# Performance work log

Hardware: AMD Instinct MI355X
Metric: run time of the kernel (lower is better)

## Reference

```python
import jax, jax.numpy as jnp
import numpy as np

N_NODES = 50000
N_EDGES = 500000
IN_DIM = 256
HIDDEN = 128
HEADS = 4
N_CLS = 10
N_GRAPHS = 512
NEG_SLOPE = 0.2  # PyG GATConv default leaky-relu slope


def _glorot(key, shape):
    fan_in, fan_out = shape[0], shape[-1]
    lim = jnp.sqrt(6.0 / (fan_in + fan_out))
    return jax.random.uniform(key, shape, jnp.float32, -lim, lim)


def setup_inputs() -> dict:
    key = jax.random.key(0)
    ks = jax.random.split(key, 12)
    x = jax.random.normal(ks[0], (N_NODES, IN_DIM), jnp.float32)
    edge_index = jax.random.randint(ks[1], (2, N_EDGES), 0, N_NODES, jnp.int64)
    batch = jnp.sort(jax.random.randint(ks[2], (N_NODES,), 0, N_GRAPHS, jnp.int64))
    HC = HIDDEN * HEADS
    return {
        "x": x,
        "edge_index": edge_index,
        "batch": batch,
        "W1": _glorot(ks[3], (IN_DIM, HC)),
        "a_src1": _glorot(ks[4], (HEADS, HIDDEN)) * 0.1,
        "a_dst1": _glorot(ks[5], (HEADS, HIDDEN)) * 0.1,
        "b1": jnp.zeros((HC,), jnp.float32),
        "W2": _glorot(ks[6], (HC, HC)),
        "a_src2": _glorot(ks[7], (HEADS, HIDDEN)) * 0.1,
        "a_dst2": _glorot(ks[8], (HEADS, HIDDEN)) * 0.1,
        "b2": jnp.zeros((HC,), jnp.float32),
        "Wc": _glorot(ks[9], (HC, N_CLS)),
        "bc": jnp.zeros((N_CLS,), jnp.float32),
    }


def _gat_layer(x, src, dst, W, a_src, a_dst, b):
    """PyG GATConv (concat=True, self-loops already appended, eval mode)."""
    N = x.shape[0]
    h = (x @ W).reshape(N, HEADS, -1)                 # [N, H, C]
    alpha_s = jnp.einsum('nhc,hc->nh', h, a_src)       # [N, H]
    alpha_d = jnp.einsum('nhc,hc->nh', h, a_dst)       # [N, H]
    e = jax.nn.leaky_relu(alpha_s[src] + alpha_d[dst], NEG_SLOPE)  # [E, H]
    # segment softmax over incoming edges of each dst node
    m = jax.ops.segment_max(e, dst, num_segments=N)
    ex = jnp.exp(e - m[dst])
    denom = jax.ops.segment_sum(ex, dst, num_segments=N)
    alpha = ex / (denom[dst] + 1e-16)                  # [E, H]
    out = jax.ops.segment_sum(alpha[:, :, None] * h[src], dst, num_segments=N)
    return out.reshape(N, -1) + b                      # [N, H*C]


def reference(x, edge_index, batch, W1, a_src1, a_dst1, b1,
              W2, a_src2, a_dst2, b2, Wc, bc):
    N = x.shape[0]
    loop = jnp.arange(N, dtype=edge_index.dtype)
    src = jnp.concatenate([edge_index[0], loop])
    dst = jnp.concatenate([edge_index[1], loop])
    h = jax.nn.relu(_gat_layer(x, src, dst, W1, a_src1, a_dst1, b1))
    h = jax.nn.relu(_gat_layer(h, src, dst, W2, a_src2, a_dst2, b2))
    # global mean pool over graphs
    sums = jax.ops.segment_sum(h, batch, num_segments=N_GRAPHS)
    cnt = jax.ops.segment_sum(jnp.ones((N,), h.dtype), batch, num_segments=N_GRAPHS)
    hg = sums / jnp.maximum(cnt, 1.0)[:, None]         # [G, H*C]
    return hg @ Wc + bc                                # [G, n_cls]
```

## Files before the change

kernel.cpp:

```cpp
#include <hip/hip_runtime.h>

#define NN      50000
#define NE      500000
#define NET     550000
#define IND     256
#define HC      512
#define NH      4
#define NG      512
#define NCLS    10

typedef __attribute__((ext_vector_type(8))) _Float16 f16x8;
typedef __attribute__((ext_vector_type(4))) float f32x4;
typedef __attribute__((ext_vector_type(2))) float f32x2;
typedef __attribute__((ext_vector_type(4))) ushort us4;

__device__ __forceinline__ ushort f2bf(float x) {
    unsigned u = __float_as_uint(x);
    u += 0x7fffu + ((u >> 16) & 1u);
    return (ushort)(u >> 16);
}
__device__ __forceinline__ float bf2f(ushort h) {
    return __uint_as_float((unsigned)h << 16);
}
__device__ __forceinline__ ushort f2h(float x) {
    union { _Float16 h; ushort u; } cv;
    cv.h = (_Float16)x;
    return cv.u;
}
__device__ __forceinline__ float h2f(ushort u) {
    union { ushort u; _Float16 h; } cv;
    cv.u = u;
    return (float)cv.h;
}

__device__ __forceinline__ void gload_lds16(const void* g, void* s) {
    __builtin_amdgcn_global_load_lds(
        (const __attribute__((address_space(1))) unsigned*)g,
        (__attribute__((address_space(3))) unsigned*)s, 16, 0, 0);
}

__global__ __launch_bounds__(256) void k_gemm_f16(
    const ushort* __restrict__ A, const ushort* __restrict__ BT,
    const float* __restrict__ a_srcv, const float* __restrict__ a_dstv,
    unsigned char* __restrict__ Cf8, float* __restrict__ as_b,
    float* __restrict__ ad_b, int M, int K)
{
    __shared__ __align__(16) ushort As[64 * 64];
    __shared__ __align__(16) ushort Bs[128 * 64];
    __shared__ float sred[2][64];

    const int tid = threadIdx.x;
    const int nwg = gridDim.x;
    const int orig = blockIdx.x;
    const int q = nwg >> 3, r = nwg & 7, xcd = orig & 7;
    const int wgid = (xcd < r ? xcd * (q + 1) : r * (q + 1) + (xcd - r) * q) + (orig >> 3);
    const int bm = (wgid >> 2) * 64;
    const int bn = (wgid & 3) * 128;

    const int l = tid & 63;
    const int w = tid >> 6;
    const int wm = (w >> 1) * 32, wn = (w & 1) * 64;
    const int fr = l & 15;
    const int fk = (l >> 4) * 8;

    if (tid < 64) { sred[0][tid] = 0.f; sred[1][tid] = 0.f; }

    f32x4 zero = {0.f, 0.f, 0.f, 0.f};
    f32x4 acc[2][4];
#pragma unroll
    for (int m = 0; m < 2; ++m)
#pragma unroll
        for (int n = 0; n < 4; ++n) acc[m][n] = zero;

    const int nsteps = K >> 6;
    const int wbase = (tid & 0xC0) << 4;

    for (int ks = 0; ks < nsteps; ++ks) {
        int k0 = ks << 6;
#pragma unroll
        for (int i = 0; i < 2; ++i) {
            int c = i * 256 + tid;
            int row = c >> 3;
            int col16 = (c & 7) ^ (row & 7);
            int arow = bm + row; arow = arow < M ? arow : M - 1;
            gload_lds16(A + (size_t)arow * K + k0 + (col16 << 3),
                        (char*)As + i * 4096 + wbase);
        }
#pragma unroll
        for (int i = 0; i < 4; ++i) {
            int c = i * 256 + tid;
            int j = c >> 3;
            int col16 = (c & 7) ^ (j & 7);
            gload_lds16(BT + (size_t)(bn + j) * K + k0 + (col16 << 3),
                        (char*)Bs + i * 4096 + wbase);
        }
        __syncthreads();
#pragma unroll
        for (int kk = 0; kk < 64; kk += 32) {
            f16x8 a[2], b[4];
            int kb = (kk + fk) >> 3;
#pragma unroll
            for (int m = 0; m < 2; ++m) {
                int row = wm + m * 16 + fr;
                a[m] = *(const f16x8*)((const char*)As + row * 128 + ((kb ^ (row & 7)) << 4));
            }
#pragma unroll
            for (int n = 0; n < 4; ++n) {
                int col = wn + n * 16 + fr;
                b[n] = *(const f16x8*)((const char*)Bs + col * 128 + ((kb ^ (col & 7)) << 4));
            }
#pragma unroll
            for (int m = 0; m < 2; ++m)
#pragma unroll
                for (int n = 0; n < 4; ++n)
                    acc[m][n] = __builtin_amdgcn_mfma_f32_16x16x32_f16(a[m], b[n], acc[m][n], 0, 0, 0);
        }
        __syncthreads();
    }

    const int hh = bn >> 7;
    float asl[4], adl[4];
#pragma unroll
    for (int n = 0; n < 4; ++n) {
        int c = wn + n * 16 + fr;
        asl[n] = a_srcv[hh * 128 + c];
        adl[n] = a_dstv[hh * 128 + c];
    }
    const int rbase = (l >> 4) * 4;
#pragma unroll
    for (int m = 0; m < 2; ++m) {
#pragma unroll
        for (int rr = 0; rr < 4; ++rr) {
            int rloc = wm + m * 16 + rbase + rr;
            int rowi = bm + rloc;
            float ps = 0.f, pd = 0.f;
#pragma unroll
            for (int n = 0; n < 4; ++n) {
                float v = acc[m][n][rr];
                ps += v * asl[n];
                pd += v * adl[n];
                if (rowi < M) {
                    int pk = __builtin_amdgcn_cvt_pk_fp8_f32(v, v, 0, false);
                    Cf8[(size_t)rowi * HC + bn + wn + n * 16 + fr] = (unsigned char)pk;
                }
            }
#pragma unroll
            for (int off = 1; off < 16; off <<= 1) {
                ps += __shfl_xor(ps, off, 64);
                pd += __shfl_xor(pd, off, 64);
            }
            if (fr == 0) {
                atomicAdd(&sred[0][rloc], ps);
                atomicAdd(&sred[1][rloc], pd);
            }
        }
    }
    __syncthreads();
    if (tid < 64) {
        int rowi = bm + tid;
        if (rowi < M) {
            as_b[rowi * 4 + hh] = sred[0][tid];
            ad_b[rowi * 4 + hh] = sred[1][tid];
        }
    }
}

__global__ void k_cvt_f16(const float* __restrict__ in, ushort* __restrict__ o,
                          int n4) {
    int i = blockIdx.x * blockDim.x + threadIdx.x;
    if (i >= n4) return;
    float4 v = ((const float4*)in)[i];
    ushort4 h;
    h.x = f2h(v.x); h.y = f2h(v.y); h.z = f2h(v.z); h.w = f2h(v.w);
    ((ushort4*)o)[i] = h;
}

__global__ void k_cvt_wT(const float* __restrict__ W, ushort* __restrict__ hT,
                         int K, int logK) {
    int id = blockIdx.x * blockDim.x + threadIdx.x;
    if (id >= (HC << logK)) return;
    int nn = id >> logK, k = id & (K - 1);
    hT[id] = f2h(W[(size_t)k * HC + nn]);
}

__global__ void k_deg(const int* __restrict__ ei, int* __restrict__ deg) {
    int e = blockIdx.x * blockDim.x + threadIdx.x;
    if (e >= NET) return;
    int d = (e < NE) ? ei[NE + e] : (e - NE);
    atomicAdd(&deg[d], 1);
}

__global__ __launch_bounds__(256) void k_scan_part(const int* __restrict__ cnt,
                                                   int* __restrict__ bsum, int n) {
    __shared__ int red[256];
    const int tid = threadIdx.x;
    int i = blockIdx.x * 256 + tid;
    red[tid] = (i < n) ? cnt[i] : 0;
    __syncthreads();
#pragma unroll
    for (int d = 128; d; d >>= 1) {
        if (tid < d) red[tid] += red[tid + d];
        __syncthreads();
    }
    if (tid == 0) bsum[blockIdx.x] = red[0];
}

__global__ __launch_bounds__(1024) void k_scan_top(const int* __restrict__ bsum,
                                                   int* __restrict__ boff,
                                                   int* __restrict__ off, int nb, int n) {
    __shared__ int s[1024];
    const int tid = threadIdx.x;
    int v = (tid < nb) ? bsum[tid] : 0;
    s[tid] = v;
    __syncthreads();
    for (int d = 1; d < 1024; d <<= 1) {
        int t = (tid >= d) ? s[tid - d] : 0;
        __syncthreads();
        s[tid] += t;
        __syncthreads();
    }
    if (tid < nb) boff[tid] = s[tid] - v;
    if (tid == nb - 1) off[n] = s[tid];
}

__global__ __launch_bounds__(256) void k_scan_out(const int* __restrict__ cnt,
                                                  const int* __restrict__ boff,
                                                  int* __restrict__ off, int n) {
    __shared__ int s[256];
    const int tid = threadIdx.x;
    int i = blockIdx.x * 256 + tid;
    int v = (i < n) ? cnt[i] : 0;
    s[tid] = v;
    __syncthreads();
    for (int d = 1; d < 256; d <<= 1) {
        int t = (tid >= d) ? s[tid - d] : 0;
        __syncthreads();
        s[tid] += t;
        __syncthreads();
    }
    if (i < n) off[i] = boff[blockIdx.x] + s[tid] - v;
}

__global__ void k_fill(const int* __restrict__ ei,
                       const int* __restrict__ rowptr,
                       int* __restrict__ fillcnt,
                       ushort* __restrict__ colsrc) {
    int e = blockIdx.x * blockDim.x + threadIdx.x;
    if (e >= NET) return;
    int s, d;
    if (e < NE) { s = ei[e]; d = ei[NE + e]; } else { s = d = e - NE; }
    int pos = rowptr[d] + atomicAdd(&fillcnt[d], 1);
    colsrc[pos] = (ushort)s;
}

__global__ __launch_bounds__(256) void k_stats(
    const float* __restrict__ as, const float* __restrict__ ad,
    const int* __restrict__ rowptr, const ushort* __restrict__ colsrc,
    ushort* __restrict__ alpha, float* __restrict__ dinv, int N)
{
    const int n = blockIdx.x * 64 + (threadIdx.x >> 2);
    if (n >= N) return;
    const int h = threadIdx.x & 3;
    const int beg = rowptr[n], end = rowptr[n + 1];
    const float adn = ad[n * 4 + h];
    float sum = 0.f;
    for (int e = beg; e < end; ++e) {
        float ev = as[(int)colsrc[e] * 4 + h] + adn;
        ev = ev > 0.f ? ev : 0.2f * ev;
        float a = __expf(ev);
        alpha[(size_t)e * 4 + h] = f2h(a);
        sum += a;
    }
    dinv[n * 4 + h] = 1.0f / (sum + 1e-16f);
}

__global__ __launch_bounds__(256) void k_gather(
    const unsigned char* __restrict__ zf8, const ushort* __restrict__ alpha,
    const float* __restrict__ dinv, const int* __restrict__ rowptr,
    const ushort* __restrict__ colsrc, const float* __restrict__ bias,
    ushort* __restrict__ o16, int obf16)
{
    const int npb = NN >> 2;
    const int hp = blockIdx.x / npb;
    const int sub = threadIdx.x >> 5;
    const int node = (blockIdx.x % npb) * 4 + (sub >> 1);
    const int head = hp * 2 + (sub & 1);
    const int lane = threadIdx.x & 31;
    const int beg = rowptr[node], end = rowptr[node + 1];
    const unsigned char* __restrict__ zh = zf8 + head * 128 + (lane << 2);

    float ax = 0.f, ay = 0.f, az = 0.f, aw = 0.f;
    int e = beg;
    for (; e + 8 <= end; e += 8) {
        int s[8];
        float a[8];
        unsigned u[8];
#pragma unroll
        for (int j = 0; j < 8; ++j) {
            s[j] = colsrc[e + j];
            a[j] = h2f(alpha[(size_t)(e + j) * 4 + head]);
        }
#pragma unroll
        for (int j = 0; j < 8; ++j) u[j] = *(const unsigned*)&zh[(size_t)s[j] * HC];
#pragma unroll
        for (int j = 0; j < 8; ++j) {
            f32x2 lo = __builtin_amdgcn_cvt_pk_f32_fp8(u[j], false);
            f32x2 hi = __builtin_amdgcn_cvt_pk_f32_fp8(u[j], true);
            ax += a[j] * lo.x; ay += a[j] * lo.y;
            az += a[j] * hi.x; aw += a[j] * hi.y;
        }
    }
    for (; e + 2 <= end; e += 2) {
        int s0 = colsrc[e], s1 = colsrc[e + 1];
        float a0 = h2f(alpha[(size_t)e * 4 + head]);
        float a1 = h2f(alpha[(size_t)(e + 1) * 4 + head]);
        unsigned u0 = *(const unsigned*)&zh[(size_t)s0 * HC];
        unsigned u1 = *(const unsigned*)&zh[(size_t)s1 * HC];
        f32x2 l0 = __builtin_amdgcn_cvt_pk_f32_fp8(u0, false);
        f32x2 h0 = __builtin_amdgcn_cvt_pk_f32_fp8(u0, true);
        f32x2 l1 = __builtin_amdgcn_cvt_pk_f32_fp8(u1, false);
        f32x2 h1 = __builtin_amdgcn_cvt_pk_f32_fp8(u1, true);
        ax += a0 * l0.x + a1 * l1.x; ay += a0 * l0.y + a1 * l1.y;
        az += a0 * h0.x + a1 * h1.x; aw += a0 * h0.y + a1 * h1.y;
    }
    if (e < end) {
        int s0 = colsrc[e];
        float a0 = h2f(alpha[(size_t)e * 4 + head]);
        unsigned u0 = *(const unsigned*)&zh[(size_t)s0 * HC];
        f32x2 l0 = __builtin_amdgcn_cvt_pk_f32_fp8(u0, false);
        f32x2 h0 = __builtin_amdgcn_cvt_pk_f32_fp8(u0, true);
        ax += a0 * l0.x; ay += a0 * l0.y; az += a0 * h0.x; aw += a0 * h0.y;
    }
    const float di = dinv[node * 4 + head];
    const int col = head * 128 + (lane << 2);
    float4 bv = *(const float4*)&bias[col];
    float rx = fmaxf(ax * di + bv.x, 0.f), ry = fmaxf(ay * di + bv.y, 0.f);
    float rz = fmaxf(az * di + bv.z, 0.f), rw = fmaxf(aw * di + bv.w, 0.f);
    us4 h;
    if (obf16) {
        h.x = f2bf(rx); h.y = f2bf(ry); h.z = f2bf(rz); h.w = f2bf(rw);
    } else {
        h.x = f2h(rx); h.y = f2h(ry); h.z = f2h(rz); h.w = f2h(rw);
    }
    __builtin_nontemporal_store(h, (us4*)&o16[(size_t)node * HC + col]);
}

__global__ void k_gcnt(const int* __restrict__ batch, int* __restrict__ gcnt) {
    int n = blockIdx.x * blockDim.x + threadIdx.x;
    if (n < NN) atomicAdd(&gcnt[batch[n]], 1);
}

__global__ __launch_bounds__(128) void k_pool(const ushort* __restrict__ h,
                                              const int* __restrict__ goff,
                                              const int* __restrict__ gcnt,
                                              float* __restrict__ hg) {
    const int g = blockIdx.x;
    const int tid = threadIdx.x;
    const int beg = goff[g];
    const int cnt = gcnt[g];
    float4 acc = make_float4(0.f, 0.f, 0.f, 0.f);
    for (int r = beg; r < beg + cnt; ++r) {
        ushort4 v = *(const ushort4*)&h[(size_t)r * HC + (tid << 2)];
        acc.x += bf2f(v.x); acc.y += bf2f(v.y);
        acc.z += bf2f(v.z); acc.w += bf2f(v.w);
    }
    float inv = 1.0f / (float)max(cnt, 1);
    *(float4*)&hg[(size_t)g * HC + (tid << 2)] =
        make_float4(acc.x * inv, acc.y * inv, acc.z * inv, acc.w * inv);
}

__global__ __launch_bounds__(64) void k_cls(const float* __restrict__ hg,
                                            const float* __restrict__ Wc,
                                            const float* __restrict__ bc,
                                            float* __restrict__ out) {
    const int g = blockIdx.x;
    const int lane = threadIdx.x;
#pragma unroll 1
    for (int cls = 0; cls < NCLS; ++cls) {
        float p = 0.f;
#pragma unroll
        for (int j = 0; j < 8; ++j) {
            int c = lane + j * 64;
            p += hg[(size_t)g * HC + c] * Wc[c * NCLS + cls];
        }
#pragma unroll
        for (int off = 32; off; off >>= 1) p += __shfl_down(p, off, 64);
        if (lane == 0) out[g * NCLS + cls] = p + bc[cls];
    }
}

extern "C" void kernel_launch(void* const* d_in, const int* in_sizes, int n_in,
                              void* d_out, int out_size, void* d_ws, size_t ws_size,
                              hipStream_t stream) {
    const float* x     = (const float*)d_in[0];
    const int*   ei    = (const int*)d_in[1];
    const int*   batch = (const int*)d_in[2];
    const float* W1    = (const float*)d_in[3];
    const float* asrc1 = (const float*)d_in[4];
    const float* adst1 = (const float*)d_in[5];
    const float* b1    = (const float*)d_in[6];
    const float* W2    = (const float*)d_in[7];
    const float* asrc2 = (const float*)d_in[8];
    const float* adst2 = (const float*)d_in[9];
    const float* b2    = (const float*)d_in[10];
    const float* Wc    = (const float*)d_in[11];
    const float* bc    = (const float*)d_in[12];
    float* out = (float*)d_out;
    (void)in_sizes; (void)n_in; (void)out_size; (void)ws_size;

    char* R = (char*)d_ws;
    const size_t MB512 = (size_t)NN * HC;
    unsigned char* zf8 = (unsigned char*)R;
    ushort* xf16  = (ushort*)(R + MB512);
    ushort* h1f16 = (ushort*)(R + MB512);
    ushort* h2b   = (ushort*)(R + MB512);

    char* w = R + MB512 * 3;
    size_t off = 0;
    auto alloc = [&](size_t bytes) {
        void* p = w + off;
        off += (bytes + 255) & ~(size_t)255;
        return p;
    };
    float* as_b = (float*)alloc((size_t)NN * NH * 4);
    float* ad_b = (float*)alloc((size_t)NN * NH * 4);
    float* dinv = (float*)alloc((size_t)NN * NH * 4);
    int* rowptr = (int*)alloc((size_t)(NN + 1) * 4);
    int* deg    = (int*)alloc((size_t)NN * 4);
    ushort* colsrc = (ushort*)alloc((size_t)NET * 2);
    int* gcnt   = (int*)alloc((size_t)NG * 4);
    int* goff   = (int*)alloc((size_t)(NG + 1) * 4);
    int* bsum   = (int*)alloc((size_t)1024 * 4);
    int* boff   = (int*)alloc((size_t)1024 * 4);
    float* hg   = (float*)alloc((size_t)NG * HC * 4);
    ushort* W1T = (ushort*)alloc((size_t)HC * IND * 2);
    ushort* W2T = (ushort*)alloc((size_t)HC * HC * 2);
    ushort* alpha = (ushort*)alloc((size_t)NET * NH * 2);

    const int EB = 256, EG = (NET + EB - 1) / EB;
    const int MT = (NN + 63) / 64;
    const int GG = 2 * (NN >> 2);
    const int NB_N = (NN + 255) / 256;
    const int NB_G = (NG + 255) / 256;

    k_cvt_f16<<<(NN * IND / 4 + 255) / 256, 256, 0, stream>>>(x, xf16, NN * IND / 4);
    k_cvt_wT<<<(HC * IND + 255) / 256, 256, 0, stream>>>(W1, W1T, IND, 8);
    k_cvt_wT<<<(HC * HC + 255) / 256, 256, 0, stream>>>(W2, W2T, HC, 9);

    hipMemsetAsync(deg, 0, (size_t)NN * 4, stream);
    k_deg<<<EG, EB, 0, stream>>>(ei, deg);
    k_scan_part<<<NB_N, 256, 0, stream>>>(deg, bsum, NN);
    k_scan_top<<<1, 1024, 0, stream>>>(bsum, boff, rowptr, NB_N, NN);
    k_scan_out<<<NB_N, 256, 0, stream>>>(deg, boff, rowptr, NN);
    hipMemsetAsync(deg, 0, (size_t)NN * 4, stream);
    k_fill<<<EG, EB, 0, stream>>>(ei, rowptr, deg, colsrc);

    hipMemsetAsync(gcnt, 0, (size_t)NG * 4, stream);
    k_gcnt<<<(NN + 255) / 256, 256, 0, stream>>>(batch, gcnt);
    k_scan_part<<<NB_G, 256, 0, stream>>>(gcnt, bsum, NG);
    k_scan_top<<<1, 1024, 0, stream>>>(bsum, boff, goff, NB_G, NG);
    k_scan_out<<<NB_G, 256, 0, stream>>>(gcnt, boff, goff, NG);

    k_gemm_f16<<<MT * 4, 256, 0, stream>>>(xf16, W1T, asrc1, adst1,
                                           zf8, as_b, ad_b, NN, IND);
    k_stats<<<(NN + 63) / 64, 256, 0, stream>>>(as_b, ad_b, rowptr, colsrc,
                                                alpha, dinv, NN);
    k_gather<<<GG, 256, 0, stream>>>(zf8, alpha, dinv, rowptr, colsrc, b1,
                                     h1f16, 0);

    k_gemm_f16<<<MT * 4, 256, 0, stream>>>(h1f16, W2T, asrc2, adst2,
                                           zf8, as_b, ad_b, NN, HC);
    k_stats<<<(NN + 63) / 64, 256, 0, stream>>>(as_b, ad_b, rowptr, colsrc,
                                                alpha, dinv, NN);
    k_gather<<<GG, 256, 0, stream>>>(zf8, alpha, dinv, rowptr, colsrc, b2,
                                     h2b, 1);

    k_pool<<<NG, 128, 0, stream>>>(h2b, goff, gcnt, hg);
    k_cls<<<NG, 64, 0, stream>>>(hg, Wc, bc, out);
}
```

Before: 394.2 us.

## Double-buffer GEMM LDS tiles and fuse small preprocessing kernels

The GEMM now double-buffers its A/B LDS tiles, issuing the next k-step's global-to-LDS loads before computing the current one and replacing __syncthreads with an explicit vmcnt wait plus barrier. Separately, the three conversion kernels are merged into one launch, the degree and graph-count atomics are merged into one kernel, and the graph offset scan uses a single-block 512-thread scan instead of the three-kernel scan. Together these aim to hide global load latency in the GEMM and cut kernel launch overhead. The cost is doubled LDS per block, which may lower occupancy, and the vmcnt(0) wait only partially overlaps the loads with compute.

```diff
diff --git a/kernel.cpp b/kernel.cpp
--- a/kernel.cpp
+++ b/kernel.cpp
@@ -45,8 +45,8 @@
     unsigned char* __restrict__ Cf8, float* __restrict__ as_b,
     float* __restrict__ ad_b, int M, int K)
 {
-    __shared__ __align__(16) ushort As[64 * 64];
-    __shared__ __align__(16) ushort Bs[128 * 64];
+    __shared__ __align__(16) ushort As[2][64 * 64];
+    __shared__ __align__(16) ushort Bs[2][128 * 64];
     __shared__ float sred[2][64];
 
     const int tid = threadIdx.x;
@@ -75,7 +75,7 @@
     const int nsteps = K >> 6;
     const int wbase = (tid & 0xC0) << 4;
 
-    for (int ks = 0; ks < nsteps; ++ks) {
+    auto stage = [&](int buf, int ks) {
         int k0 = ks << 6;
 #pragma unroll
         for (int i = 0; i < 2; ++i) {
@@ -84,7 +84,7 @@
             int col16 = (c & 7) ^ (row & 7);
             int arow = bm + row; arow = arow < M ? arow : M - 1;
             gload_lds16(A + (size_t)arow * K + k0 + (col16 << 3),
-                        (char*)As + i * 4096 + wbase);
+                        (char*)As[buf] + i * 4096 + wbase);
         }
 #pragma unroll
         for (int i = 0; i < 4; ++i) {
@@ -92,9 +92,17 @@
             int j = c >> 3;
             int col16 = (c & 7) ^ (j & 7);
             gload_lds16(BT + (size_t)(bn + j) * K + k0 + (col16 << 3),
-                        (char*)Bs + i * 4096 + wbase);
-        }
-        __syncthreads();
+                        (char*)Bs[buf] + i * 4096 + wbase);
+        }
+    };
+
+    stage(0, 0);
+    asm volatile("s_waitcnt vmcnt(0)" ::: "memory");
+    __builtin_amdgcn_s_barrier();
+
+    for (int ks = 0; ks < nsteps; ++ks) {
+        const int cur = ks & 1;
+        if (ks + 1 < nsteps) stage(cur ^ 1, ks + 1);
 #pragma unroll
         for (int kk = 0; kk < 64; kk += 32) {
             f16x8 a[2], b[4];
@@ -102,12 +110,12 @@
 #pragma unroll
             for (int m = 0; m < 2; ++m) {
                 int row = wm + m * 16 + fr;
-                a[m] = *(const f16x8*)((const char*)As + row * 128 + ((kb ^ (row & 7)) << 4));
+                a[m] = *(const f16x8*)((const char*)As[cur] + row * 128 + ((kb ^ (row & 7)) << 4));
             }
 #pragma unroll
             for (int n = 0; n < 4; ++n) {
                 int col = wn + n * 16 + fr;
-                b[n] = *(const f16x8*)((const char*)Bs + col * 128 + ((kb ^ (col & 7)) << 4));
+                b[n] = *(const f16x8*)((const char*)Bs[cur] + col * 128 + ((kb ^ (col & 7)) << 4));
             }
 #pragma unroll
             for (int m = 0; m < 2; ++m)
@@ -115,7 +123,8 @@
                 for (int n = 0; n < 4; ++n)
                     acc[m][n] = __builtin_amdgcn_mfma_f32_16x16x32_f16(a[m], b[n], acc[m][n], 0, 0, 0);
         }
-        __syncthreads();
+        asm volatile("s_waitcnt vmcnt(0)" ::: "memory");
+        __builtin_amdgcn_s_barrier();
     }
 
     const int hh = bn >> 7;
@@ -165,29 +174,43 @@
     }
 }
 
-__global__ void k_cvt_f16(const float* __restrict__ in, ushort* __restrict__ o,
-                          int n4) {
+#define CVT_X4   (NN * IND / 4)
+#define CVT_W1   (HC * IND)
+#define CVT_W2   (HC * HC)
+__global__ void k_cvt_all(const float* __restrict__ x, ushort* __restrict__ xf16,
+                          const float* __restrict__ W1, ushort* __restrict__ W1T,
+                          const float* __restrict__ W2, ushort* __restrict__ W2T) {
     int i = blockIdx.x * blockDim.x + threadIdx.x;
-    if (i >= n4) return;
-    float4 v = ((const float4*)in)[i];
-    ushort4 h;
-    h.x = f2h(v.x); h.y = f2h(v.y); h.z = f2h(v.z); h.w = f2h(v.w);
-    ((ushort4*)o)[i] = h;
-}
-
-__global__ void k_cvt_wT(const float* __restrict__ W, ushort* __restrict__ hT,
-                         int K, int logK) {
-    int id = blockIdx.x * blockDim.x + threadIdx.x;
-    if (id >= (HC << logK)) return;
-    int nn = id >> logK, k = id & (K - 1);
-    hT[id] = f2h(W[(size_t)k * HC + nn]);
-}
-
-__global__ void k_deg(const int* __restrict__ ei, int* __restrict__ deg) {
-    int e = blockIdx.x * blockDim.x + threadIdx.x;
-    if (e >= NET) return;
-    int d = (e < NE) ? ei[NE + e] : (e - NE);
-    atomicAdd(&deg[d], 1);
+    if (i < CVT_X4) {
+        float4 v = ((const float4*)x)[i];
+        ushort4 h;
+        h.x = f2h(v.x); h.y = f2h(v.y); h.z = f2h(v.z); h.w = f2h(v.w);
+        ((ushort4*)xf16)[i] = h;
+        return;
+    }
+    i -= CVT_X4;
+    if (i < CVT_W1) {
+        int nn = i >> 8, k = i & 255;
+        W1T[i] = f2h(W1[(size_t)k * HC + nn]);
+        return;
+    }
+    i -= CVT_W1;
+    if (i < CVT_W2) {
+        int nn = i >> 9, k = i & 511;
+        W2T[i] = f2h(W2[(size_t)k * HC + nn]);
+    }
+}
+
+__global__ void k_count(const int* __restrict__ ei, int* __restrict__ deg,
+                        const int* __restrict__ batch, int* __restrict__ gcnt) {
+    int i = blockIdx.x * blockDim.x + threadIdx.x;
+    if (i < NET) {
+        int d = (i < NE) ? ei[NE + i] : (i - NE);
+        atomicAdd(&deg[d], 1);
+    } else {
+        int j = i - NET;
+        if (j < NN) atomicAdd(&gcnt[batch[j]], 1);
+    }
 }
 
 __global__ __launch_bounds__(256) void k_scan_part(const int* __restrict__ cnt,
@@ -239,6 +262,23 @@
         __syncthreads();
     }
     if (i < n) off[i] = boff[blockIdx.x] + s[tid] - v;
+}
+
+__global__ __launch_bounds__(512) void k_scan_small(const int* __restrict__ cnt,
+                                                    int* __restrict__ off, int n) {
+    __shared__ int s[512];
+    const int tid = threadIdx.x;
+    int v = (tid < n) ? cnt[tid] : 0;
+    s[tid] = v;
+    __syncthreads();
+    for (int d = 1; d < 512; d <<= 1) {
+        int t = (tid >= d) ? s[tid - d] : 0;
+        __syncthreads();
+        s[tid] += t;
+        __syncthreads();
+    }
+    if (tid < n) off[tid] = s[tid] - v;
+    if (tid == n - 1) off[n] = s[tid];
 }
 
 __global__ void k_fill(const int* __restrict__ ei,
@@ -345,19 +385,13 @@
     __builtin_nontemporal_store(h, (us4*)&o16[(size_t)node * HC + col]);
 }
 
-__global__ void k_gcnt(const int* __restrict__ batch, int* __restrict__ gcnt) {
-    int n = blockIdx.x * blockDim.x + threadIdx.x;
-    if (n < NN) atomicAdd(&gcnt[batch[n]], 1);
-}
-
 __global__ __launch_bounds__(128) void k_pool(const ushort* __restrict__ h,
                                               const int* __restrict__ goff,
-                                              const int* __restrict__ gcnt,
                                               float* __restrict__ hg) {
     const int g = blockIdx.x;
     const int tid = threadIdx.x;
     const int beg = goff[g];
-    const int cnt = gcnt[g];
+    const int cnt = goff[g + 1] - beg;
     float4 acc = make_float4(0.f, 0.f, 0.f, 0.f);
     for (int r = beg; r < beg + cnt; ++r) {
         ushort4 v = *(const ushort4*)&h[(size_t)r * HC + (tid << 2)];
@@ -441,25 +475,20 @@
     const int MT = (NN + 63) / 64;
     const int GG = 2 * (NN >> 2);
     const int NB_N = (NN + 255) / 256;
-    const int NB_G = (NG + 255) / 256;
-
-    k_cvt_f16<<<(NN * IND / 4 + 255) / 256, 256, 0, stream>>>(x, xf16, NN * IND / 4);
-    k_cvt_wT<<<(HC * IND + 255) / 256, 256, 0, stream>>>(W1, W1T, IND, 8);
-    k_cvt_wT<<<(HC * HC + 255) / 256, 256, 0, stream>>>(W2, W2T, HC, 9);
+    const int CVT_TOTAL = CVT_X4 + CVT_W1 + CVT_W2;
+
+    k_cvt_all<<<(CVT_TOTAL + 255) / 256, 256, 0, stream>>>(x, xf16, W1, W1T, W2, W2T);
 
     hipMemsetAsync(deg, 0, (size_t)NN * 4, stream);
-    k_deg<<<EG, EB, 0, stream>>>(ei, deg);
+    hipMemsetAsync(gcnt, 0, (size_t)NG * 4, stream);
+    k_count<<<(NET + NN + 255) / 256, 256, 0, stream>>>(ei, deg, batch, gcnt);
+
     k_scan_part<<<NB_N, 256, 0, stream>>>(deg, bsum, NN);
     k_scan_top<<<1, 1024, 0, stream>>>(bsum, boff, rowptr, NB_N, NN);
     k_scan_out<<<NB_N, 256, 0, stream>>>(deg, boff, rowptr, NN);
+    k_scan_small<<<1, 512, 0, stream>>>(gcnt, goff, NG);
     hipMemsetAsync(deg, 0, (size_t)NN * 4, stream);
     k_fill<<<EG, EB, 0, stream>>>(ei, rowptr, deg, colsrc);
-
-    hipMemsetAsync(gcnt, 0, (size_t)NG * 4, stream);
-    k_gcnt<<<(NN + 255) / 256, 256, 0, stream>>>(batch, gcnt);
-    k_scan_part<<<NB_G, 256, 0, stream>>>(gcnt, bsum, NG);
-    k_scan_top<<<1, 1024, 0, stream>>>(bsum, boff, goff, NB_G, NG);
-    k_scan_out<<<NB_G, 256, 0, stream>>>(gcnt, boff, goff, NG);
 
     k_gemm_f16<<<MT * 4, 256, 0, stream>>>(xf16, W1T, asrc1, adst1,
                                            zf8, as_b, ad_b, NN, IND);
@@ -475,6 +504,6 @@
     k_gather<<<GG, 256, 0, stream>>>(zf8, alpha, dinv, rowptr, colsrc, b2,
                                      h2b, 1);
 
-    k_pool<<<NG, 128, 0, stream>>>(h2b, goff, gcnt, hg);
+    k_pool<<<NG, 128, 0, stream>>>(h2b, goff, hg);
     k_cls<<<NG, 64, 0, stream>>>(hg, Wc, bc, out);
 }
```

After: 401.6 us. No clear change (+1.9%).
